# Optimization experiments

Hardware: AMD Instinct MI355X
Metric: run time of the kernel (lower is better)

The kernel has to match this reference:

```python
import jax, jax.numpy as jnp
import numpy as np

HQ, HK, DH = 32, 8, 64
ROPE_BASE = 10000.0


def _rope_tables(T, dtype):
    pos = jnp.arange(T, dtype=jnp.float32)
    inv_freq = 1.0 / (ROPE_BASE ** (jnp.arange(0, DH, 2, dtype=jnp.float32) / DH))
    freqs = pos[:, None] * inv_freq[None, :]          # (T, DH/2)
    cos = jnp.concatenate([jnp.cos(freqs), jnp.cos(freqs)], -1).astype(dtype)  # (T, DH)
    sin = jnp.concatenate([jnp.sin(freqs), jnp.sin(freqs)], -1).astype(dtype)
    return cos, sin


def _rotate_half(t):
    return jnp.concatenate([-t[..., DH // 2:], t[..., :DH // 2]], -1)


def setup_inputs() -> dict:
    key = jax.random.key(0)
    k1, k2, k3, k4 = jax.random.split(key, 4)
    B, T, D = 2, 2048, 2048
    std = 0.02 / np.sqrt(24)
    kv_std = std / np.sqrt(HQ / HK)
    return {
        "x": jax.random.normal(k1, (B, T, D), jnp.float32),
        "Wq": jax.random.normal(k2, (D, HQ * DH), jnp.float32) * std,
        "Wkv": jax.random.normal(k3, (D, 2 * HK * DH), jnp.float32) * kv_std,
        "Wo": jax.random.normal(k4, (HQ * DH, D), jnp.float32) * std,
    }


def reference(x, Wq, Wkv, Wo):
    B, T, D = x.shape
    g = HQ // HK
    scale = DH ** -0.5
    # projections
    q = (x @ Wq).reshape(B, T, HQ, DH).transpose(0, 2, 1, 3)       # (B,Hq,T,Dh)
    kv = (x @ Wkv).reshape(B, T, 2, HK, DH)
    k = kv[:, :, 0].transpose(0, 2, 1, 3)                           # (B,Hk,T,Dh)
    v = kv[:, :, 1].transpose(0, 2, 1, 3)
    # GQA expand: each kv head repeated g times consecutively
    k = jnp.repeat(k, g, axis=1)                                    # (B,Hq,T,Dh)
    v = jnp.repeat(v, g, axis=1)
    # RoPE on q and repeated k
    cos, sin = _rope_tables(T, x.dtype)
    q = q * cos + _rotate_half(q) * sin
    k = k * cos + _rotate_half(k) * sin
    # attention
    scores = jnp.einsum('bhqd,bhkd->bhqk', q, k) * scale            # (B,Hq,T,T)
    causal = jnp.triu(jnp.ones((T, T), bool), 1)
    scores = jnp.where(causal, -jnp.inf, scores)
    attn = jax.nn.softmax(scores.astype(jnp.float32), axis=-1).astype(x.dtype)
    out = jnp.einsum('bhqk,bhkd->bhqd', attn, v)                    # (B,Hq,T,Dh)
    out = out.transpose(0, 2, 1, 3).reshape(B, T, HQ * DH)
    return out @ Wo
```

## Files before the change

kernel.cpp:

```cpp
#include <hip/hip_runtime.h>
#include <hip/hip_bf16.h>

#define DEVI __device__ __forceinline__

typedef __attribute__((ext_vector_type(4))) float f32x4;
typedef __attribute__((ext_vector_type(16))) float f32x16;
typedef __attribute__((ext_vector_type(8))) short s16x8;
typedef __attribute__((ext_vector_type(4))) short s16x4;

DEVI ushort f2bf(float f) {
  union { float f; unsigned u; } v; v.f = f;
  unsigned r = v.u + 0x7FFFu + ((v.u >> 16) & 1u);
  return (ushort)(r >> 16);
}

DEVI void gload_lds16(const void* g, void* l) {
  __builtin_amdgcn_global_load_lds((const __attribute__((address_space(1))) void*)g,
                                   (__attribute__((address_space(3))) void*)l, 16, 0, 0);
}

#define MFMA16 __builtin_amdgcn_mfma_f32_16x16x32_bf16
#define SBAR() __builtin_amdgcn_s_barrier()
#define LGKM0() asm volatile("s_waitcnt lgkmcnt(0)")

DEVI void stage128(const ushort* __restrict__ gsrc, int K, ushort* ld, int tid) {
  #pragma unroll
  for (int j = 0; j < 2; ++j) {
    const int ci = j * 512 + tid;
    const int row = ci >> 3, c = ci & 7;
    gload_lds16(gsrc + (size_t)row * K + ((c ^ (row & 7)) << 3),
                ld + (size_t)(j * 512 + (tid & ~63)) * 8);
  }
}

DEVI s16x8 ldfrag(const ushort* tile, int row, int kc) {
  return *(const s16x8*)((const char*)tile + row * 128 + ((kc ^ (row & 7)) << 4));
}

__global__ __launch_bounds__(256) void cast_bf16_k(const float* __restrict__ in,
                                                   ushort* __restrict__ out, int n) {
  int i = (blockIdx.x * 256 + threadIdx.x) * 4;
  if (i >= n) return;
  float4 v = *(const float4*)(in + i);
  ushort4 o;
  o.x = f2bf(v.x); o.y = f2bf(v.y); o.z = f2bf(v.z); o.w = f2bf(v.w);
  *(ushort4*)(out + i) = o;
}

__global__ __launch_bounds__(256) void transpose_cast_k(const float* __restrict__ in,
                                                        ushort* __restrict__ out, int R, int C) {
  __shared__ ushort tile[64][66];
  const int r0 = blockIdx.y * 64, c0 = blockIdx.x * 64;
  const int tid = threadIdx.x;
  #pragma unroll
  for (int j = 0; j < 16; ++j) {
    int idx = j * 256 + tid;
    int r = idx >> 6, c = idx & 63;
    tile[c][r] = f2bf(in[(size_t)(r0 + r) * C + c0 + c]);
  }
  __syncthreads();
  #pragma unroll
  for (int j = 0; j < 16; ++j) {
    int idx = j * 256 + tid;
    int c = idx >> 6, r = idx & 63;
    out[(size_t)(c0 + c) * R + r0 + r] = tile[c][r];
  }
}

__global__ __launch_bounds__(256) void rope_table_k(float2* __restrict__ tab) {
  int idx = blockIdx.x * 256 + threadIdx.x;
  int t = idx >> 5, i = idx & 31;
  float inv = expf(-(float)i * 0.28782313662425575f);
  float ang = (float)t * inv;
  tab[idx] = make_float2(cosf(ang), sinf(ang));
}

DEVI void kloop_2ph(const ushort* __restrict__ A, const ushort* __restrict__ BT,
                    ushort* Asm, ushort* Bsm, int m0, int n0, int K, int NKT,
                    f32x4 (&acc)[4][4], int tid, int wm, int wn, int g, int l15) {
  stage128(A + (size_t)m0 * K, K, Asm, tid);
  stage128(BT + (size_t)n0 * K, K, Bsm, tid);
  stage128(BT + (size_t)(n0 + 128) * K, K, Bsm + 8192, tid);
  stage128(BT + (size_t)n0 * K + 64, K, Bsm + 16384, tid);
  stage128(BT + (size_t)(n0 + 128) * K + 64, K, Bsm + 16384 + 8192, tid);
  asm volatile("s_waitcnt vmcnt(4)");
  SBAR();

  #pragma unroll 1
  for (int t = 0; t < NKT; ++t) {
    const ushort* Ah = Asm + (t & 1) * 8192;
    const ushort* Bh = Bsm + (t & 1) * 16384;
    s16x8 af[4][2], bfr[4][2];

    #pragma unroll
    for (int ks = 0; ks < 2; ++ks) {
      #pragma unroll
      for (int ni = 0; ni < 4; ++ni)
        bfr[ni][ks] = ldfrag(Bh, wn * 64 + ni * 16 + l15, ks * 4 + g);
      #pragma unroll
      for (int mi = 0; mi < 4; ++mi)
        af[mi][ks] = ldfrag(Ah, wm * 64 + mi * 16 + l15, ks * 4 + g);
    }
    SBAR();
    LGKM0();
    __builtin_amdgcn_sched_barrier(0);
    __builtin_amdgcn_s_setprio(1);
    #pragma unroll
    for (int mi = 0; mi < 4; ++mi)
      #pragma unroll
      for (int ni = 0; ni < 2; ++ni)
        #pragma unroll
        for (int ks = 0; ks < 2; ++ks)
          acc[mi][ni] = MFMA16(af[mi][ks], bfr[ni][ks], acc[mi][ni], 0, 0, 0);
    __builtin_amdgcn_s_setprio(0);
    SBAR();

    if (t + 1 < NKT)
      stage128(A + (size_t)m0 * K + (t + 1) * 64, K, Asm + ((t + 1) & 1) * 8192, tid);
    if (t + 2 < NKT) {
      stage128(BT + (size_t)n0 * K + (t + 2) * 64, K, Bsm + (t & 1) * 16384, tid);
      stage128(BT + (size_t)(n0 + 128) * K + (t + 2) * 64, K, Bsm + (t & 1) * 16384 + 8192, tid);
    }
    __builtin_amdgcn_s_setprio(1);
    #pragma unroll
    for (int mi = 0; mi < 4; ++mi)
      #pragma unroll
      for (int ni = 0; ni < 2; ++ni)
        #pragma unroll
        for (int ks = 0; ks < 2; ++ks)
          acc[mi][2 + ni] = MFMA16(af[mi][ks], bfr[2 + ni][ks], acc[mi][2 + ni], 0, 0, 0);
    __builtin_amdgcn_s_setprio(0);
    if (t + 2 < NKT)      asm volatile("s_waitcnt vmcnt(4)");
    else if (t + 1 < NKT) asm volatile("s_waitcnt vmcnt(0)");
    SBAR();
  }
}

__global__ __launch_bounds__(512) void gemm_qkv_w2(const ushort* __restrict__ A,
                                                   const ushort* __restrict__ BT,
                                                   const float2* __restrict__ tab,
                                                   ushort* __restrict__ Qp,
                                                   ushort* __restrict__ Kp,
                                                   ushort* __restrict__ Vp) {
  constexpr int K = 2048, NKT = 32, GX = 12, NWG = 384;
  __shared__ __attribute__((aligned(128))) ushort smem[49152];
  ushort* Asm = smem;
  ushort* Bsm = smem + 16384;

  const int tid = threadIdx.x;
  const int ln = tid & 63, wv = tid >> 6;
  const int g = ln >> 4, l15 = ln & 15, l31 = ln & 31, hi = ln >> 5;
  const int wm = wv >> 2, wn = wv & 3;

  const int orig = blockIdx.x;
  const int wg = (orig & 7) * (NWG / 8) + (orig >> 3);
  const int bx = wg % GX, by = wg / GX;
  const int m0 = by * 128, n0 = bx * 256;

  f32x4 acc[4][4];
  #pragma unroll
  for (int i = 0; i < 4; ++i)
    #pragma unroll
    for (int j = 0; j < 4; ++j) acc[i][j] = (f32x4){0.f, 0.f, 0.f, 0.f};

  kloop_2ph(A, BT, Asm, Bsm, m0, n0, K, NKT, acc, tid, wm, wn, g, l15);

  const int bq = by >> 4;
  const int tb0 = (by & 15) * 128;
  const int type = (bx < 8) ? 0 : (bx < 10 ? 1 : 2);
  constexpr int OST = 260;
  ushort* Ot = smem;

  __syncthreads();
  #pragma unroll
  for (int mi = 0; mi < 4; ++mi)
    #pragma unroll
    for (int r = 0; r < 4; ++r) {
      const int tl = wm * 64 + mi * 16 + g * 4 + r;
      const int t = tb0 + tl;
      #pragma unroll
      for (int ni = 0; ni < 4; ++ni) {
        const int cl = wn * 64 + ni * 16 + l15;
        float val = acc[mi][ni][r], outv;
        if (type < 2) {
          float pairv = acc[mi][ni ^ 2][r];
          float2 cs = tab[t * 32 + (ni & 1) * 16 + l15];
          outv = (ni & 2) ? (val * cs.x + pairv * cs.y) : (val * cs.x - pairv * cs.y);
          if (type == 0) outv *= 0.18033688011112042f;
        } else {
          outv = val;
        }
        Ot[tl * OST + cl] = f2bf(outv);
      }
    }
  __syncthreads();

  #pragma unroll
  for (int it = 0; it < 8; ++it) {
    const int id = wv * 8 + it;
    const int hl = id >> 4, q4 = (id >> 2) & 3, fi = id & 3;
    const int tile = (by & 15) * 4 + q4;
    if (type < 2) {
      const ushort* srow = Ot + (q4 * 32 + l31) * OST + hl * 64 + fi * 16 + hi * 8;
      union { s16x4 h[2]; s16x8 v; } u;
      u.h[0] = *(const s16x4*)srow;
      u.h[1] = *(const s16x4*)(srow + 4);
      ushort* dst;
      if (type == 0) {
        const int h = bx * 4 + hl;
        dst = Qp + (((size_t)(bq * 32 + h) * 64 + tile) * 4 + fi) * 512 + ln * 8;
      } else {
        const int h = (bx - 8) * 4 + hl;
        dst = Kp + (((size_t)(bq * 8 + h) * 64 + tile) * 4 + fi) * 512 + ln * 8;
      }
      *(s16x8*)dst = u.v;
    } else {
      const int hk = (bx - 10) * 4 + hl;
      const int col = hl * 64 + (fi & 1) * 32 + l31;
      const int row0 = q4 * 32 + (fi >> 1) * 16 + hi * 8;
      union { ushort o[8]; s16x8 v; } u;
      #pragma unroll
      for (int j2 = 0; j2 < 8; ++j2) u.o[j2] = Ot[(row0 + j2) * OST + col];
      ushort* dst = Vp + (((size_t)(bq * 8 + hk) * 64 + tile) * 4 + fi) * 512 + ln * 8;
      *(s16x8*)dst = u.v;
    }
  }
}

__global__ __launch_bounds__(512) void gemm_wo_w2(const ushort* __restrict__ A,
                                                  const ushort* __restrict__ BT,
                                                  float* __restrict__ C) {
  constexpr int K = 2048, NKT = 32, N = 2048, GX = 8, NWG = 256;
  __shared__ __attribute__((aligned(128))) ushort smem[49152];
  ushort* Asm = smem;
  ushort* Bsm = smem + 16384;

  const int tid = threadIdx.x;
  const int ln = tid & 63, wv = tid >> 6;
  const int g = ln >> 4, l15 = ln & 15;
  const int wm = wv >> 2, wn = wv & 3;

  const int orig = blockIdx.x;
  const int wg = (orig & 7) * (NWG / 8) + (orig >> 3);
  const int bx = wg % GX, by = wg / GX;
  const int m0 = by * 128, n0 = bx * 256;

  f32x4 acc[4][4];
  #pragma unroll
  for (int i = 0; i < 4; ++i)
    #pragma unroll
    for (int j = 0; j < 4; ++j) acc[i][j] = (f32x4){0.f, 0.f, 0.f, 0.f};

  kloop_2ph(A, BT, Asm, Bsm, m0, n0, K, NKT, acc, tid, wm, wn, g, l15);

  #pragma unroll
  for (int mi = 0; mi < 4; ++mi)
    #pragma unroll
    for (int r = 0; r < 4; ++r) {
      int row = m0 + wm * 64 + mi * 16 + g * 4 + r;
      float* crow = C + (size_t)row * N + n0 + wn * 64 + l15;
      #pragma unroll
      for (int ni = 0; ni < 4; ++ni) crow[ni * 16] = acc[mi][ni][r];
    }
}

__global__ __launch_bounds__(256) void attn_k(const ushort* __restrict__ Qp,
                                              const ushort* __restrict__ Kp,
                                              const ushort* __restrict__ Vp,
                                              ushort* __restrict__ O) {
  __shared__ ushort ep[4][32 * 64];
  const int tid = threadIdx.x, wv = tid >> 6, ln = tid & 63;
  const int l31 = ln & 31, hi = ln >> 5;

  const int f = blockIdx.x + gridDim.x * (blockIdx.y + 32 * blockIdx.z);
  const int xcd = f & 7, j = f >> 3;
  const int pr = xcd + 8 * (j & 1);
  const int b = pr >> 3, hk = pr & 7;
  const int s = j >> 1;
  const int hq = hk * 4 + (s & 3);
  const int qtile = 63 - ((s >> 2) * 4 + wv);
  const int qw = qtile * 32;
  const int nt = qtile + 1;

  const ushort* Qh    = Qp + ((size_t)(b * 32 + hq)) * (64 * 2048);
  const ushort* Kbase = Kp + ((size_t)(b * 8 + hk)) * (64 * 2048);
  const ushort* Vbase = Vp + ((size_t)(b * 8 + hk)) * (64 * 2048);
  ushort* lds = ep[wv];

  s16x8 qf[4];
  {
    const ushort* qp_ = Qh + (size_t)qtile * 2048 + ln * 8;
    #pragma unroll
    for (int ks = 0; ks < 4; ++ks) qf[ks] = *(const s16x8*)(qp_ + ks * 512);
  }

  f32x16 oacc[2];
  #pragma unroll
  for (int dt = 0; dt < 2; ++dt)
    #pragma unroll
    for (int r = 0; r < 16; ++r) oacc[dt][r] = 0.f;
  float m = -1e30f, l = 0.f;

  const ushort* kp = Kbase + ln * 8;
  const ushort* vp = Vbase + ln * 8;

  s16x8 kf[4];
  #pragma unroll
  for (int ks = 0; ks < 4; ++ks) kf[ks] = *(const s16x8*)(kp + ks * 512);
  kp += 2048;

  s16x8 vc[4];
  union pfu { unsigned u[4]; s16x8 v; };
  pfu pf0, pf1;

  #pragma unroll 1
  for (int kt = 0; kt < nt; ++kt) {
    if (kt) {
      __builtin_amdgcn_s_setprio(1);
      oacc[0] = __builtin_amdgcn_mfma_f32_32x32x16_bf16(vc[0], pf0.v, oacc[0], 0, 0, 0);
      oacc[1] = __builtin_amdgcn_mfma_f32_32x32x16_bf16(vc[1], pf0.v, oacc[1], 0, 0, 0);
      oacc[0] = __builtin_amdgcn_mfma_f32_32x32x16_bf16(vc[2], pf1.v, oacc[0], 0, 0, 0);
      oacc[1] = __builtin_amdgcn_mfma_f32_32x32x16_bf16(vc[3], pf1.v, oacc[1], 0, 0, 0);
      __builtin_amdgcn_s_setprio(0);
    }
    #pragma unroll
    for (int fi2 = 0; fi2 < 4; ++fi2) vc[fi2] = *(const s16x8*)(vp + fi2 * 512);
    vp += 2048;

    f32x16 sp;
    #pragma unroll
    for (int r = 0; r < 16; ++r) sp[r] = 0.f;
    __builtin_amdgcn_s_setprio(1);
    #pragma unroll
    for (int ks = 0; ks < 4; ++ks)
      sp = __builtin_amdgcn_mfma_f32_32x32x16_bf16(kf[ks], qf[ks], sp, 0, 0, 0);
    __builtin_amdgcn_s_setprio(0);

    if (kt + 1 < nt) {
      #pragma unroll
      for (int ks = 0; ks < 4; ++ks) kf[ks] = *(const s16x8*)(kp + ks * 512);
      kp += 2048;
    }

    if (kt == qtile) {
      #pragma unroll
      for (int r = 0; r < 16; ++r) {
        int key = (r & 3) + 8 * (r >> 2) + 4 * hi;
        if (key > l31) sp[r] = -1e30f;
      }
    }

    float t0 = fmaxf(fmaxf(sp[0], sp[1]), sp[2]);
    float t1 = fmaxf(fmaxf(sp[3], sp[4]), sp[5]);
    float t2 = fmaxf(fmaxf(sp[6], sp[7]), sp[8]);
    float t3 = fmaxf(fmaxf(sp[9], sp[10]), sp[11]);
    float t4 = fmaxf(fmaxf(sp[12], sp[13]), sp[14]);
    float u0 = fmaxf(fmaxf(t0, t1), t2);
    float u1 = fmaxf(fmaxf(t3, t4), sp[15]);
    float pm = fmaxf(u0, u1);
    pm = fmaxf(pm, __shfl_xor(pm, 32, 64));

    if (__any(pm > m)) {
      float mn = fmaxf(m, pm);
      float alpha = __builtin_amdgcn_exp2f(m - mn);
      m = mn;
      l *= alpha;
      #pragma unroll
      for (int dt = 0; dt < 2; ++dt)
        #pragma unroll
        for (int r = 0; r < 16; ++r) oacc[dt][r] *= alpha;
    }

    #pragma unroll
    for (int r = 0; r < 16; ++r) sp[r] = __builtin_amdgcn_exp2f(sp[r] - m);
    {
      float a0 = sp[0] + sp[1], a1 = sp[2] + sp[3], a2 = sp[4] + sp[5], a3 = sp[6] + sp[7];
      float a4 = sp[8] + sp[9], a5 = sp[10] + sp[11], a6 = sp[12] + sp[13], a7 = sp[14] + sp[15];
      float b0 = a0 + a1, b1 = a2 + a3, b2 = a4 + a5, b3 = a6 + a7;
      float rs = (b0 + b1) + (b2 + b3);
      rs += __shfl_xor(rs, 32, 64);
      l += rs;
    }

    unsigned cw[8], xs[8];
    #pragma unroll
    for (int jj = 0; jj < 8; ++jj) {
      union { __hip_bfloat162 h; unsigned u; } pk;
      pk.h = __float22bfloat162_rn(make_float2(sp[2 * jj], sp[2 * jj + 1]));
      cw[jj] = pk.u;
    }
    #pragma unroll
    for (int jj = 0; jj < 8; ++jj) xs[jj] = __shfl_xor(cw[jj], 32, 64);
    pf0.u[0] = hi ? xs[2] : cw[0];
    pf0.u[1] = hi ? xs[3] : cw[1];
    pf0.u[2] = hi ? cw[2] : xs[0];
    pf0.u[3] = hi ? cw[3] : xs[1];
    pf1.u[0] = hi ? xs[6] : cw[4];
    pf1.u[1] = hi ? xs[7] : cw[5];
    pf1.u[2] = hi ? cw[6] : xs[4];
    pf1.u[3] = hi ? cw[7] : xs[5];
  }

  __builtin_amdgcn_s_setprio(1);
  oacc[0] = __builtin_amdgcn_mfma_f32_32x32x16_bf16(vc[0], pf0.v, oacc[0], 0, 0, 0);
  oacc[1] = __builtin_amdgcn_mfma_f32_32x32x16_bf16(vc[1], pf0.v, oacc[1], 0, 0, 0);
  oacc[0] = __builtin_amdgcn_mfma_f32_32x32x16_bf16(vc[2], pf1.v, oacc[0], 0, 0, 0);
  oacc[1] = __builtin_amdgcn_mfma_f32_32x32x16_bf16(vc[3], pf1.v, oacc[1], 0, 0, 0);
  __builtin_amdgcn_s_setprio(0);

  float invl = 1.0f / l;
  #pragma unroll
  for (int dt = 0; dt < 2; ++dt)
    #pragma unroll
    for (int r = 0; r < 16; ++r) {
      int d = dt * 32 + (r & 3) + 8 * (r >> 2) + 4 * hi;
      int byte = (l31 * 128 + d * 2) ^ ((l31 & 7) << 4);
      *(ushort*)((char*)lds + byte) = f2bf(oacc[dt][r] * invl);
    }
  const int qr = ln >> 1, half = ln & 1;
  #pragma unroll
  for (int jj = 0; jj < 4; ++jj) {
    int byte = (qr * 128 + half * 64 + jj * 16) ^ ((qr & 7) << 4);
    s16x8 vrow = *(const s16x8*)((const char*)lds + byte);
    *(s16x8*)(O + ((size_t)(b * 2048 + qw + qr)) * 2048 + hq * 64 + half * 32 + jj * 8) = vrow;
  }
}

extern "C" void kernel_launch(void* const* d_in, const int* in_sizes, int n_in,
                              void* d_out, int out_size, void* d_ws, size_t ws_size,
                              hipStream_t stream) {
  const float* x   = (const float*)d_in[0];
  const float* Wq  = (const float*)d_in[1];
  const float* Wkv = (const float*)d_in[2];
  const float* Wo  = (const float*)d_in[3];
  float* out = (float*)d_out;

  char* ws = (char*)d_ws;
  ushort* xb     = (ushort*)(ws);
  ushort* WqkvT  = (ushort*)(ws + 16777216);
  ushort* WoT    = (ushort*)(ws + 29360128);
  float2* tab    = (float2*)(ws + 37748736);
  ushort* Qp     = (ushort*)(ws + 38273024);
  ushort* Kp     = (ushort*)(ws + 55050240);
  ushort* Vp     = (ushort*)(ws + 59244544);
  ushort* Ob     = (ushort*)(ws + 63438848);

  cast_bf16_k<<<8192, 256, 0, stream>>>(x, xb, 2 * 2048 * 2048);
  transpose_cast_k<<<dim3(32, 32), 256, 0, stream>>>(Wq, WqkvT, 2048, 2048);
  transpose_cast_k<<<dim3(16, 32), 256, 0, stream>>>(Wkv, WqkvT + 2048 * 2048, 2048, 1024);
  transpose_cast_k<<<dim3(32, 32), 256, 0, stream>>>(Wo, WoT, 2048, 2048);
  rope_table_k<<<256, 256, 0, stream>>>(tab);
  gemm_qkv_w2<<<384, 512, 0, stream>>>(xb, WqkvT, tab, Qp, Kp, Vp);
  attn_k<<<dim3(16, 32, 2), 256, 0, stream>>>(Qp, Kp, Vp, Ob);
  gemm_wo_w2<<<256, 512, 0, stream>>>(Ob, WoT, out);
}
```

Before: 235.5 us.

## Shrink GEMM tiles to 128x128 with 4-wave workgroups and drop XCD remap

Both the QKV projection and the output projection GEMMs go from 128x256 tiles with 8 waves (512 threads) to 128x128 tiles with 4 waves (256 threads). The staging helper is rewritten for 256 threads and the B double buffer shrinks, cutting LDS to 64KB per block. This doubles the block count so more blocks can be resident per CU and tail effects change, but it lowers per-block data reuse. The chiplet-aware block-index remap is removed, which may hurt L2 locality.

Result: no change. 232.0 us (-1.5%).

```diff
diff --git a/kernel.cpp b/kernel.cpp
--- a/kernel.cpp
+++ b/kernel.cpp
@@ -23,18 +23,75 @@
 #define SBAR() __builtin_amdgcn_s_barrier()
 #define LGKM0() asm volatile("s_waitcnt lgkmcnt(0)")
 
-DEVI void stage128(const ushort* __restrict__ gsrc, int K, ushort* ld, int tid) {
-  #pragma unroll
-  for (int j = 0; j < 2; ++j) {
-    const int ci = j * 512 + tid;
+DEVI void stage128q(const ushort* __restrict__ gsrc, int K, ushort* ld, int tid) {
+  #pragma unroll
+  for (int j = 0; j < 4; ++j) {
+    const int ci = j * 256 + tid;
     const int row = ci >> 3, c = ci & 7;
     gload_lds16(gsrc + (size_t)row * K + ((c ^ (row & 7)) << 3),
-                ld + (size_t)(j * 512 + (tid & ~63)) * 8);
+                ld + (size_t)(j * 256 + (tid & ~63)) * 8);
   }
 }
 
 DEVI s16x8 ldfrag(const ushort* tile, int row, int kc) {
   return *(const s16x8*)((const char*)tile + row * 128 + ((kc ^ (row & 7)) << 4));
+}
+
+DEVI void kloop2(const ushort* __restrict__ A, const ushort* __restrict__ BT,
+                 ushort* Asm, ushort* Bsm, int m0, int n0, int K, int NKT,
+                 f32x4 (&acc)[4][4], int tid, int wm, int wn, int g, int l15) {
+  stage128q(A + (size_t)m0 * K, K, Asm, tid);
+  stage128q(BT + (size_t)n0 * K, K, Bsm, tid);
+  stage128q(BT + (size_t)n0 * K + 64, K, Bsm + 8192, tid);
+  asm volatile("s_waitcnt vmcnt(4)");
+  SBAR();
+
+  #pragma unroll 1
+  for (int t = 0; t < NKT; ++t) {
+    const ushort* Ah = Asm + (t & 1) * 8192;
+    const ushort* Bh = Bsm + (t & 1) * 8192;
+    s16x8 af[4][2], bfr[4][2];
+
+    #pragma unroll
+    for (int ks = 0; ks < 2; ++ks) {
+      #pragma unroll
+      for (int ni = 0; ni < 4; ++ni)
+        bfr[ni][ks] = ldfrag(Bh, wn * 64 + ni * 16 + l15, ks * 4 + g);
+      #pragma unroll
+      for (int mi = 0; mi < 4; ++mi)
+        af[mi][ks] = ldfrag(Ah, wm * 64 + mi * 16 + l15, ks * 4 + g);
+    }
+    SBAR();
+    LGKM0();
+    __builtin_amdgcn_sched_barrier(0);
+    __builtin_amdgcn_s_setprio(1);
+    #pragma unroll
+    for (int mi = 0; mi < 4; ++mi)
+      #pragma unroll
+      for (int ni = 0; ni < 2; ++ni)
+        #pragma unroll
+        for (int ks = 0; ks < 2; ++ks)
+          acc[mi][ni] = MFMA16(af[mi][ks], bfr[ni][ks], acc[mi][ni], 0, 0, 0);
+    __builtin_amdgcn_s_setprio(0);
+    SBAR();
+
+    if (t + 1 < NKT)
+      stage128q(A + (size_t)m0 * K + (t + 1) * 64, K, Asm + ((t + 1) & 1) * 8192, tid);
+    if (t + 2 < NKT)
+      stage128q(BT + (size_t)n0 * K + (t + 2) * 64, K, Bsm + (t & 1) * 8192, tid);
+    __builtin_amdgcn_s_setprio(1);
+    #pragma unroll
+    for (int mi = 0; mi < 4; ++mi)
+      #pragma unroll
+      for (int ni = 0; ni < 2; ++ni)
+        #pragma unroll
+        for (int ks = 0; ks < 2; ++ks)
+          acc[mi][2 + ni] = MFMA16(af[mi][ks], bfr[2 + ni][ks], acc[mi][2 + ni], 0, 0, 0);
+    __builtin_amdgcn_s_setprio(0);
+    if (t + 2 < NKT)      asm volatile("s_waitcnt vmcnt(4)");
+    else if (t + 1 < NKT) asm volatile("s_waitcnt vmcnt(0)");
+    SBAR();
+  }
 }
 
 __global__ __launch_bounds__(256) void cast_bf16_k(const float* __restrict__ in,
@@ -75,87 +132,23 @@
   tab[idx] = make_float2(cosf(ang), sinf(ang));
 }
 
-DEVI void kloop_2ph(const ushort* __restrict__ A, const ushort* __restrict__ BT,
-                    ushort* Asm, ushort* Bsm, int m0, int n0, int K, int NKT,
-                    f32x4 (&acc)[4][4], int tid, int wm, int wn, int g, int l15) {
-  stage128(A + (size_t)m0 * K, K, Asm, tid);
-  stage128(BT + (size_t)n0 * K, K, Bsm, tid);
-  stage128(BT + (size_t)(n0 + 128) * K, K, Bsm + 8192, tid);
-  stage128(BT + (size_t)n0 * K + 64, K, Bsm + 16384, tid);
-  stage128(BT + (size_t)(n0 + 128) * K + 64, K, Bsm + 16384 + 8192, tid);
-  asm volatile("s_waitcnt vmcnt(4)");
-  SBAR();
-
-  #pragma unroll 1
-  for (int t = 0; t < NKT; ++t) {
-    const ushort* Ah = Asm + (t & 1) * 8192;
-    const ushort* Bh = Bsm + (t & 1) * 16384;
-    s16x8 af[4][2], bfr[4][2];
-
-    #pragma unroll
-    for (int ks = 0; ks < 2; ++ks) {
-      #pragma unroll
-      for (int ni = 0; ni < 4; ++ni)
-        bfr[ni][ks] = ldfrag(Bh, wn * 64 + ni * 16 + l15, ks * 4 + g);
-      #pragma unroll
-      for (int mi = 0; mi < 4; ++mi)
-        af[mi][ks] = ldfrag(Ah, wm * 64 + mi * 16 + l15, ks * 4 + g);
-    }
-    SBAR();
-    LGKM0();
-    __builtin_amdgcn_sched_barrier(0);
-    __builtin_amdgcn_s_setprio(1);
-    #pragma unroll
-    for (int mi = 0; mi < 4; ++mi)
-      #pragma unroll
-      for (int ni = 0; ni < 2; ++ni)
-        #pragma unroll
-        for (int ks = 0; ks < 2; ++ks)
-          acc[mi][ni] = MFMA16(af[mi][ks], bfr[ni][ks], acc[mi][ni], 0, 0, 0);
-    __builtin_amdgcn_s_setprio(0);
-    SBAR();
-
-    if (t + 1 < NKT)
-      stage128(A + (size_t)m0 * K + (t + 1) * 64, K, Asm + ((t + 1) & 1) * 8192, tid);
-    if (t + 2 < NKT) {
-      stage128(BT + (size_t)n0 * K + (t + 2) * 64, K, Bsm + (t & 1) * 16384, tid);
-      stage128(BT + (size_t)(n0 + 128) * K + (t + 2) * 64, K, Bsm + (t & 1) * 16384 + 8192, tid);
-    }
-    __builtin_amdgcn_s_setprio(1);
-    #pragma unroll
-    for (int mi = 0; mi < 4; ++mi)
-      #pragma unroll
-      for (int ni = 0; ni < 2; ++ni)
-        #pragma unroll
-        for (int ks = 0; ks < 2; ++ks)
-          acc[mi][2 + ni] = MFMA16(af[mi][ks], bfr[2 + ni][ks], acc[mi][2 + ni], 0, 0, 0);
-    __builtin_amdgcn_s_setprio(0);
-    if (t + 2 < NKT)      asm volatile("s_waitcnt vmcnt(4)");
-    else if (t + 1 < NKT) asm volatile("s_waitcnt vmcnt(0)");
-    SBAR();
-  }
-}
-
-__global__ __launch_bounds__(512) void gemm_qkv_w2(const ushort* __restrict__ A,
-                                                   const ushort* __restrict__ BT,
-                                                   const float2* __restrict__ tab,
-                                                   ushort* __restrict__ Qp,
-                                                   ushort* __restrict__ Kp,
-                                                   ushort* __restrict__ Vp) {
-  constexpr int K = 2048, NKT = 32, GX = 12, NWG = 384;
-  __shared__ __attribute__((aligned(128))) ushort smem[49152];
+__global__ __launch_bounds__(256) void gemm_qkv_2ph(const ushort* __restrict__ A,
+                                                    const ushort* __restrict__ BT,
+                                                    const float2* __restrict__ tab,
+                                                    ushort* __restrict__ Qp,
+                                                    ushort* __restrict__ Kp,
+                                                    ushort* __restrict__ Vp) {
+  constexpr int K = 2048, NKT = 32;
+  __shared__ __attribute__((aligned(128))) ushort smem[32768];
   ushort* Asm = smem;
   ushort* Bsm = smem + 16384;
+  ushort* Ot = smem;
 
   const int tid = threadIdx.x;
   const int ln = tid & 63, wv = tid >> 6;
   const int g = ln >> 4, l15 = ln & 15, l31 = ln & 31, hi = ln >> 5;
-  const int wm = wv >> 2, wn = wv & 3;
-
-  const int orig = blockIdx.x;
-  const int wg = (orig & 7) * (NWG / 8) + (orig >> 3);
-  const int bx = wg % GX, by = wg / GX;
-  const int m0 = by * 128, n0 = bx * 256;
+  const int wm = wv >> 1, wn = wv & 1;
+  const int m0 = blockIdx.y * 128, n0 = blockIdx.x * 128;
 
   f32x4 acc[4][4];
   #pragma unroll
@@ -163,25 +156,24 @@
     #pragma unroll
     for (int j = 0; j < 4; ++j) acc[i][j] = (f32x4){0.f, 0.f, 0.f, 0.f};
 
-  kloop_2ph(A, BT, Asm, Bsm, m0, n0, K, NKT, acc, tid, wm, wn, g, l15);
-
-  const int bq = by >> 4;
-  const int tb0 = (by & 15) * 128;
-  const int type = (bx < 8) ? 0 : (bx < 10 ? 1 : 2);
-  constexpr int OST = 260;
-  ushort* Ot = smem;
+  kloop2(A, BT, Asm, Bsm, m0, n0, K, NKT, acc, tid, wm, wn, g, l15);
 
   __syncthreads();
+  const int bq = m0 >> 11;
+  const int tg0 = m0 & 2047;
+  const int type = (n0 < 2048) ? 0 : (n0 < 2560 ? 1 : 2);
+
   #pragma unroll
   for (int mi = 0; mi < 4; ++mi)
     #pragma unroll
     for (int r = 0; r < 4; ++r) {
       const int tl = wm * 64 + mi * 16 + g * 4 + r;
-      const int t = tb0 + tl;
+      const int t = tg0 + tl;
       #pragma unroll
       for (int ni = 0; ni < 4; ++ni) {
         const int cl = wn * 64 + ni * 16 + l15;
-        float val = acc[mi][ni][r], outv;
+        float val = acc[mi][ni][r];
+        float outv;
         if (type < 2) {
           float pairv = acc[mi][ni ^ 2][r];
           float2 cs = tab[t * 32 + (ni & 1) * 16 + l15];
@@ -190,7 +182,7 @@
         } else {
           outv = val;
         }
-        Ot[tl * OST + cl] = f2bf(outv);
+        Ot[tl * 132 + cl] = f2bf(outv);
       }
     }
   __syncthreads();
@@ -199,51 +191,47 @@
   for (int it = 0; it < 8; ++it) {
     const int id = wv * 8 + it;
     const int hl = id >> 4, q4 = (id >> 2) & 3, fi = id & 3;
-    const int tile = (by & 15) * 4 + q4;
+    const int tile = (tg0 >> 5) + q4;
     if (type < 2) {
-      const ushort* srow = Ot + (q4 * 32 + l31) * OST + hl * 64 + fi * 16 + hi * 8;
+      const ushort* srow = Ot + (q4 * 32 + l31) * 132 + hl * 64 + fi * 16 + hi * 8;
       union { s16x4 h[2]; s16x8 v; } u;
       u.h[0] = *(const s16x4*)srow;
       u.h[1] = *(const s16x4*)(srow + 4);
       ushort* dst;
       if (type == 0) {
-        const int h = bx * 4 + hl;
+        const int h = (n0 >> 6) + hl;
         dst = Qp + (((size_t)(bq * 32 + h) * 64 + tile) * 4 + fi) * 512 + ln * 8;
       } else {
-        const int h = (bx - 8) * 4 + hl;
+        const int h = ((n0 - 2048) >> 6) + hl;
         dst = Kp + (((size_t)(bq * 8 + h) * 64 + tile) * 4 + fi) * 512 + ln * 8;
       }
       *(s16x8*)dst = u.v;
     } else {
-      const int hk = (bx - 10) * 4 + hl;
+      const int hk = ((n0 - 2560) >> 6) + hl;
       const int col = hl * 64 + (fi & 1) * 32 + l31;
       const int row0 = q4 * 32 + (fi >> 1) * 16 + hi * 8;
-      union { ushort o[8]; s16x8 v; } u;
-      #pragma unroll
-      for (int j2 = 0; j2 < 8; ++j2) u.o[j2] = Ot[(row0 + j2) * OST + col];
+      ushort o[8];
+      #pragma unroll
+      for (int j = 0; j < 8; ++j) o[j] = Ot[(row0 + j) * 132 + col];
       ushort* dst = Vp + (((size_t)(bq * 8 + hk) * 64 + tile) * 4 + fi) * 512 + ln * 8;
-      *(s16x8*)dst = u.v;
-    }
-  }
-}
-
-__global__ __launch_bounds__(512) void gemm_wo_w2(const ushort* __restrict__ A,
-                                                  const ushort* __restrict__ BT,
-                                                  float* __restrict__ C) {
-  constexpr int K = 2048, NKT = 32, N = 2048, GX = 8, NWG = 256;
-  __shared__ __attribute__((aligned(128))) ushort smem[49152];
+      *(s16x8*)dst = *(const s16x8*)o;
+    }
+  }
+}
+
+__global__ __launch_bounds__(256) void gemm_bt_2ph(const ushort* __restrict__ A,
+                                                   const ushort* __restrict__ BT,
+                                                   float* __restrict__ C, int M, int N, int K) {
+  __shared__ __attribute__((aligned(128))) ushort smem[32768];
   ushort* Asm = smem;
   ushort* Bsm = smem + 16384;
 
   const int tid = threadIdx.x;
   const int ln = tid & 63, wv = tid >> 6;
   const int g = ln >> 4, l15 = ln & 15;
-  const int wm = wv >> 2, wn = wv & 3;
-
-  const int orig = blockIdx.x;
-  const int wg = (orig & 7) * (NWG / 8) + (orig >> 3);
-  const int bx = wg % GX, by = wg / GX;
-  const int m0 = by * 128, n0 = bx * 256;
+  const int wm = wv >> 1, wn = wv & 1;
+  const int m0 = blockIdx.y * 128, n0 = blockIdx.x * 128;
+  const int NKT = K / 64;
 
   f32x4 acc[4][4];
   #pragma unroll
@@ -251,7 +239,7 @@
     #pragma unroll
     for (int j = 0; j < 4; ++j) acc[i][j] = (f32x4){0.f, 0.f, 0.f, 0.f};
 
-  kloop_2ph(A, BT, Asm, Bsm, m0, n0, K, NKT, acc, tid, wm, wn, g, l15);
+  kloop2(A, BT, Asm, Bsm, m0, n0, K, NKT, acc, tid, wm, wn, g, l15);
 
   #pragma unroll
   for (int mi = 0; mi < 4; ++mi)
@@ -450,7 +438,7 @@
   transpose_cast_k<<<dim3(16, 32), 256, 0, stream>>>(Wkv, WqkvT + 2048 * 2048, 2048, 1024);
   transpose_cast_k<<<dim3(32, 32), 256, 0, stream>>>(Wo, WoT, 2048, 2048);
   rope_table_k<<<256, 256, 0, stream>>>(tab);
-  gemm_qkv_w2<<<384, 512, 0, stream>>>(xb, WqkvT, tab, Qp, Kp, Vp);
+  gemm_qkv_2ph<<<dim3(24, 32), 256, 0, stream>>>(xb, WqkvT, tab, Qp, Kp, Vp);
   attn_k<<<dim3(16, 32, 2), 256, 0, stream>>>(Qp, Kp, Vp, Ob);
-  gemm_wo_w2<<<256, 512, 0, stream>>>(Ob, WoT, out);
-}
+  gemm_bt_2ph<<<dim3(16, 32), 256, 0, stream>>>(Ob, WoT, out, 4096, 2048, 2048);
+}
```
